# Performance work log

Hardware: AMD Instinct MI355X
Metric: run time of the kernel (lower is better)

Reference implementation:

```python
import jax, jax.numpy as jnp
import numpy as np

# Intersection(mode='product'):
#   a_fk = a @ feats.T            # [Na, K]
#   b_fk = b @ feats.T            # [Nb, K]
#   mask = (a_fk[:,None,:] > 0) & (b_fk[None,:,:] > 0)
#   result = sum_k (a_fk[:,None,:] * b_fk[None,:,:]) * mask   # [Na, Nb]
# For the product op, (x*y)*[x>0 & y>0] == relu(x)*relu(y) elementwise
# (any term with a non-positive factor is zeroed either way), so the
# broadcast+mask+reduce collapses exactly into a GEMM over relu'd scores.

def setup_inputs() -> dict:
    key = jax.random.key(0)
    k1, k2, k3 = jax.random.split(key, 3)
    a = jax.random.normal(k1, (1024, 2048), dtype=jnp.float32)
    b = jax.random.normal(k2, (1024, 2048), dtype=jnp.float32)
    feats = jax.random.normal(k3, (128, 2048), dtype=jnp.float32)
    return {"a": a, "b": b, "feats": feats}

def reference(a, b, feats):
    a_fk = a @ feats.T            # [Na, K]
    b_fk = b @ feats.T            # [Nb, K]
    # masked product-intersection reduced over K; identical math to the
    # broadcast (Na, Nb, K) -> sum formulation of the torch module.
    return jnp.einsum('ak,bk->ab', jax.nn.relu(a_fk), jax.nn.relu(b_fk))
```

## Files before the change

### kernel.cpp

```cpp
#include <hip/hip_runtime.h>


typedef __attribute__((ext_vector_type(8))) __bf16 bf16x8;
typedef __attribute__((ext_vector_type(4))) __bf16 bf16x4;
typedef __attribute__((ext_vector_type(4))) float floatx4;

#define KD     2048
#define NF     128
#define NA     1024
#define NPART  8
#define KSL    256
#define FKN    (2048 * 128)

#define XSZ    (64 * 72)
#define FSZ    (128 * 72)

static __device__ inline bf16x4 cvt4(float4 u) {
    bf16x4 s;
    s[0] = (__bf16)u.x; s[1] = (__bf16)u.y; s[2] = (__bf16)u.z; s[3] = (__bf16)u.w;
    return s;
}

struct Chunk {
    float4 x[4];
    float4 f[8];
};

static __device__ inline void load_chunk(Chunk& ch, const float* xp,
                                         const float* fp, int koff) {
#pragma unroll
    for (int j = 0; j < 4; j++)
        ch.x[j] = *(const float4*)(xp + (size_t)j * 16 * KD + koff);
#pragma unroll
    for (int i = 0; i < 8; i++)
        ch.f[i] = *(const float4*)(fp + (size_t)i * 16 * KD + koff);
}

static __device__ inline void write_chunk(const Chunk& ch, __bf16* Xc, __bf16* Fc,
                                          int srow, int scol) {
#pragma unroll
    for (int j = 0; j < 4; j++)
        *(bf16x4*)&Xc[(srow + 16 * j) * 72 + scol] = cvt4(ch.x[j]);
#pragma unroll
    for (int i = 0; i < 8; i++)
        *(bf16x4*)&Fc[(srow + 16 * i) * 72 + scol] = cvt4(ch.f[i]);
}

__global__ __launch_bounds__(256) void gemm1_onebar(const float* __restrict__ A,
                                                    const float* __restrict__ B,
                                                    const float* __restrict__ F,
                                                    float* __restrict__ part) {
    __shared__ __attribute__((aligned(16))) __bf16 smem[4 * XSZ + 4 * FSZ];
    __bf16* Xs = smem;
    __bf16* Fs = smem + 4 * XSZ;

    const int t    = threadIdx.x;
    const int m0   = blockIdx.x * 64;
    const int s    = blockIdx.y;
    const int k0   = s * KSL;
    const float* src = (m0 < NA) ? (A + (size_t)m0 * KD)
                                 : (B + (size_t)(m0 - NA) * KD);

    const int lane = t & 63;
    const int w    = t >> 6;
    const int ln   = lane & 15;
    const int quad = lane >> 4;
    const int q8   = quad * 8;

    const int srow = t >> 4;
    const int scol = (t & 15) * 4;
    const float* xp = src + (size_t)srow * KD + (k0 + scol);
    const float* fp = F   + (size_t)srow * KD + (k0 + scol);

    Chunk ca, cb;
    load_chunk(ca, xp, fp, 0);
    load_chunk(cb, xp, fp, 64);
    write_chunk(ca, Xs + 0 * XSZ, Fs + 0 * FSZ, srow, scol);
    load_chunk(ca, xp, fp, 128);
    write_chunk(cb, Xs + 1 * XSZ, Fs + 1 * FSZ, srow, scol);
    load_chunk(cb, xp, fp, 192);
    write_chunk(ca, Xs + 2 * XSZ, Fs + 2 * FSZ, srow, scol);
    write_chunk(cb, Xs + 3 * XSZ, Fs + 3 * FSZ, srow, scol);
    __syncthreads();

    floatx4 acc[4][2];
#pragma unroll
    for (int mt = 0; mt < 4; mt++)
#pragma unroll
        for (int nt = 0; nt < 2; nt++)
            acc[mt][nt] = (floatx4){0.f, 0.f, 0.f, 0.f};

#pragma unroll
    for (int c = 0; c < 4; c++) {
        const __bf16* Xc = Xs + c * XSZ;
        const __bf16* Fc = Fs + c * FSZ;
#pragma unroll
        for (int sub = 0; sub < 64; sub += 32) {
            bf16x8 bfrag[2];
#pragma unroll
            for (int nt = 0; nt < 2; nt++)
                bfrag[nt] = *(const bf16x8*)&Fc[(w * 32 + nt * 16 + ln) * 72 + sub + q8];
#pragma unroll
            for (int mt = 0; mt < 4; mt++) {
                bf16x8 af = *(const bf16x8*)&Xc[(mt * 16 + ln) * 72 + sub + q8];
#pragma unroll
                for (int nt = 0; nt < 2; nt++)
                    acc[mt][nt] = __builtin_amdgcn_mfma_f32_16x16x32_bf16(
                        af, bfrag[nt], acc[mt][nt], 0, 0, 0);
            }
        }
    }

    float* pdst = part + (size_t)s * FKN;
#pragma unroll
    for (int mt = 0; mt < 4; mt++)
#pragma unroll
        for (int nt = 0; nt < 2; nt++)
#pragma unroll
            for (int r = 0; r < 4; r++) {
                int row = m0 + mt * 16 + quad * 4 + r;
                int col = w * 32 + nt * 16 + ln;
                pdst[(size_t)row * NF + col] = acc[mt][nt][r];
            }
}

__global__ __launch_bounds__(256) void reduce_relu(const float* __restrict__ part,
                                                   __bf16* __restrict__ fkb) {
    int idx = blockIdx.x * 256 + threadIdx.x;
    size_t base = (size_t)idx * 4;
    float4 sum = make_float4(0.f, 0.f, 0.f, 0.f);
#pragma unroll
    for (int s = 0; s < NPART; s++) {
        float4 u = *(const float4*)(part + (size_t)s * FKN + base);
        sum.x += u.x; sum.y += u.y; sum.z += u.z; sum.w += u.w;
    }
    bf16x4 o;
    o[0] = (__bf16)fmaxf(sum.x, 0.f);
    o[1] = (__bf16)fmaxf(sum.y, 0.f);
    o[2] = (__bf16)fmaxf(sum.z, 0.f);
    o[3] = (__bf16)fmaxf(sum.w, 0.f);
    *(bf16x4*)(fkb + base) = o;
}

__global__ __launch_bounds__(256) void gemm2(const __bf16* __restrict__ fkb,
                                             float* __restrict__ out) {
    __shared__ __bf16 Ps[64 * 136];
    __shared__ __bf16 Qs[64 * 136];

    const int t    = threadIdx.x;
    const int i0   = blockIdx.y * 64;
    const int j0   = blockIdx.x * 64;
    const int lane = t & 63;
    const int w    = t >> 6;
    const int wm   = w & 1;
    const int wn   = w >> 1;
    const int ln   = lane & 15;
    const int quad = lane >> 4;
    const int q8   = quad * 8;

    const int prow = t >> 2, pcol = (t & 3) * 32;
    {
        const __bf16* p = fkb + (size_t)(i0 + prow) * NF + pcol;
        const __bf16* q = fkb + (size_t)(NA + j0 + prow) * NF + pcol;
#pragma unroll
        for (int c = 0; c < 32; c += 8) {
            *(bf16x8*)&Ps[prow * 136 + pcol + c] = *(const bf16x8*)(p + c);
            *(bf16x8*)&Qs[prow * 136 + pcol + c] = *(const bf16x8*)(q + c);
        }
    }
    __syncthreads();

    floatx4 acc[2][2];
#pragma unroll
    for (int mt = 0; mt < 2; mt++)
#pragma unroll
        for (int nt = 0; nt < 2; nt++)
            acc[mt][nt] = (floatx4){0.f, 0.f, 0.f, 0.f};

#pragma unroll
    for (int k0 = 0; k0 < 128; k0 += 32) {
        bf16x8 af[2], bf[2];
#pragma unroll
        for (int mt = 0; mt < 2; mt++)
            af[mt] = *(const bf16x8*)&Ps[(wm * 32 + mt * 16 + ln) * 136 + k0 + q8];
#pragma unroll
        for (int nt = 0; nt < 2; nt++)
            bf[nt] = *(const bf16x8*)&Qs[(wn * 32 + nt * 16 + ln) * 136 + k0 + q8];
#pragma unroll
        for (int mt = 0; mt < 2; mt++)
#pragma unroll
            for (int nt = 0; nt < 2; nt++)
                acc[mt][nt] = __builtin_amdgcn_mfma_f32_16x16x32_bf16(
                    af[mt], bf[nt], acc[mt][nt], 0, 0, 0);
    }

#pragma unroll
    for (int mt = 0; mt < 2; mt++)
#pragma unroll
        for (int nt = 0; nt < 2; nt++)
#pragma unroll
            for (int r = 0; r < 4; r++) {
                int row = i0 + wm * 32 + mt * 16 + quad * 4 + r;
                int col = j0 + wn * 32 + nt * 16 + ln;
                out[(size_t)row * 1024 + col] = acc[mt][nt][r];
            }
}

extern "C" void kernel_launch(void* const* d_in, const int* in_sizes, int n_in,
                              void* d_out, int out_size, void* d_ws, size_t ws_size,
                              hipStream_t stream) {
    const float* a     = (const float*)d_in[0];
    const float* b     = (const float*)d_in[1];
    const float* feats = (const float*)d_in[2];
    float* out = (float*)d_out;

    float*   part = (float*)d_ws;
    __bf16*  fkb  = (__bf16*)((char*)d_ws + (size_t)NPART * FKN * 4);

    gemm1_onebar<<<dim3(32, NPART), 256, 0, stream>>>(a, b, feats, part);
    reduce_relu<<<256, 256, 0, stream>>>(part, fkb);
    gemm2<<<dim3(16, 16), 256, 0, stream>>>(fkb, out);
}
```

Before: 77.91 us.

## Fuse split-K reduction and relu into gemm1 via last-block atomic counter

```diff
diff --git a/kernel.cpp b/kernel.cpp
--- a/kernel.cpp
+++ b/kernel.cpp
@@ -4,6 +4,7 @@
 typedef __attribute__((ext_vector_type(8))) __bf16 bf16x8;
 typedef __attribute__((ext_vector_type(4))) __bf16 bf16x4;
 typedef __attribute__((ext_vector_type(4))) float floatx4;
+typedef unsigned long long u64;
 
 #define KD     2048
 #define NF     128
@@ -15,12 +16,28 @@
 #define XSZ    (64 * 72)
 #define FSZ    (128 * 72)
 
+__device__ int g_ctr[32];
+
 static __device__ inline bf16x4 cvt4(float4 u) {
     bf16x4 s;
     s[0] = (__bf16)u.x; s[1] = (__bf16)u.y; s[2] = (__bf16)u.z; s[3] = (__bf16)u.w;
     return s;
 }
 
+static __device__ inline void llc_store(float* p, float v) {
+    __hip_atomic_store(p, v, __ATOMIC_RELAXED, __HIP_MEMORY_SCOPE_AGENT);
+}
+static __device__ inline float4 llc_load4(const float* p) {
+    u64 lo = __hip_atomic_load((const u64*)p,     __ATOMIC_RELAXED, __HIP_MEMORY_SCOPE_AGENT);
+    u64 hi = __hip_atomic_load((const u64*)p + 1, __ATOMIC_RELAXED, __HIP_MEMORY_SCOPE_AGENT);
+    float4 v;
+    v.x = __uint_as_float((unsigned)(lo & 0xffffffffu));
+    v.y = __uint_as_float((unsigned)(lo >> 32));
+    v.z = __uint_as_float((unsigned)(hi & 0xffffffffu));
+    v.w = __uint_as_float((unsigned)(hi >> 32));
+    return v;
+}
+
 struct Chunk {
     float4 x[4];
     float4 f[8];
@@ -46,11 +63,13 @@
         *(bf16x4*)&Fc[(srow + 16 * i) * 72 + scol] = cvt4(ch.f[i]);
 }
 
-__global__ __launch_bounds__(256) void gemm1_onebar(const float* __restrict__ A,
-                                                    const float* __restrict__ B,
-                                                    const float* __restrict__ F,
-                                                    float* __restrict__ part) {
+__global__ __launch_bounds__(256) void gemm1_onebar_red(const float* __restrict__ A,
+                                                        const float* __restrict__ B,
+                                                        const float* __restrict__ F,
+                                                        float* __restrict__ part,
+                                                        __bf16* __restrict__ fkb) {
     __shared__ __attribute__((aligned(16))) __bf16 smem[4 * XSZ + 4 * FSZ];
+    __shared__ int s_old;
     __bf16* Xs = smem;
     __bf16* Fs = smem + 4 * XSZ;
 
@@ -120,26 +139,40 @@
             for (int r = 0; r < 4; r++) {
                 int row = m0 + mt * 16 + quad * 4 + r;
                 int col = w * 32 + nt * 16 + ln;
-                pdst[(size_t)row * NF + col] = acc[mt][nt][r];
-            }
-}
-
-__global__ __launch_bounds__(256) void reduce_relu(const float* __restrict__ part,
-                                                   __bf16* __restrict__ fkb) {
-    int idx = blockIdx.x * 256 + threadIdx.x;
-    size_t base = (size_t)idx * 4;
-    float4 sum = make_float4(0.f, 0.f, 0.f, 0.f);
-#pragma unroll
-    for (int s = 0; s < NPART; s++) {
-        float4 u = *(const float4*)(part + (size_t)s * FKN + base);
-        sum.x += u.x; sum.y += u.y; sum.z += u.z; sum.w += u.w;
-    }
-    bf16x4 o;
-    o[0] = (__bf16)fmaxf(sum.x, 0.f);
-    o[1] = (__bf16)fmaxf(sum.y, 0.f);
-    o[2] = (__bf16)fmaxf(sum.z, 0.f);
-    o[3] = (__bf16)fmaxf(sum.w, 0.f);
-    *(bf16x4*)(fkb + base) = o;
+                llc_store(&pdst[(size_t)row * NF + col], acc[mt][nt][r]);
+            }
+
+    __syncthreads();
+    if (t == 0)
+        s_old = __hip_atomic_fetch_add(&g_ctr[blockIdx.x], 1,
+                                       __ATOMIC_RELAXED, __HIP_MEMORY_SCOPE_AGENT);
+    __syncthreads();
+
+    if (s_old == NPART - 1) {
+        asm volatile("" ::: "memory");
+#pragma unroll
+        for (int jj = 0; jj < 8; jj++) {
+            const int g    = jj * 256 + t;
+            const int row  = g >> 5;
+            const int col4 = (g & 31) * 4;
+            const float* p = part + (size_t)(m0 + row) * NF + col4;
+            float4 sum = make_float4(0.f, 0.f, 0.f, 0.f);
+#pragma unroll
+            for (int s2 = 0; s2 < NPART; s2++) {
+                float4 u = llc_load4(p + (size_t)s2 * FKN);
+                sum.x += u.x; sum.y += u.y; sum.z += u.z; sum.w += u.w;
+            }
+            bf16x4 o;
+            o[0] = (__bf16)fmaxf(sum.x, 0.f);
+            o[1] = (__bf16)fmaxf(sum.y, 0.f);
+            o[2] = (__bf16)fmaxf(sum.z, 0.f);
+            o[3] = (__bf16)fmaxf(sum.w, 0.f);
+            *(bf16x4*)(fkb + (size_t)(m0 + row) * NF + col4) = o;
+        }
+        if (t == 0)
+            __hip_atomic_store(&g_ctr[blockIdx.x], 0,
+                               __ATOMIC_RELAXED, __HIP_MEMORY_SCOPE_AGENT);
+    }
 }
 
 __global__ __launch_bounds__(256) void gemm2(const __bf16* __restrict__ fkb,
@@ -217,7 +250,6 @@
     float*   part = (float*)d_ws;
     __bf16*  fkb  = (__bf16*)((char*)d_ws + (size_t)NPART * FKN * 4);
 
-    gemm1_onebar<<<dim3(32, NPART), 256, 0, stream>>>(a, b, feats, part);
-    reduce_relu<<<256, 256, 0, stream>>>(part, fkb);
+    gemm1_onebar_red<<<dim3(32, NPART), 256, 0, stream>>>(a, b, feats, part, fkb);
     gemm2<<<dim3(16, 16), 256, 0, stream>>>(fkb, out);
 }
```

Result: slower. 81.06 us (+4.0%).
